# Optimization experiments

Measured on AMD Instinct MI355X. Metric: run time of the kernel, lower is better.

## Reference

```python
import jax, jax.numpy as jnp
import numpy as np

EMBED_DIM = 512
NUM_HEADS = 8
NUM_LAYERS = 2
LN_EPS = 1e-5


def setup_inputs() -> dict:
    key = jax.random.key(0)
    ks = jax.random.split(key, 12)
    B, S, E, L = 8, 1024, EMBED_DIM, NUM_LAYERS
    scale = 1.0 / np.sqrt(E)  # kaiming-ish init scale for 1x1 conv weights
    return {
        "x": jax.random.normal(ks[0], (B, S, E), jnp.float32),
        "adj": jax.random.uniform(ks[1], (S, S), jnp.float32),
        "Wq": jax.random.normal(ks[2], (L, E, E), jnp.float32) * scale,
        "bq": jnp.zeros((L, E), jnp.float32),
        "Wk": jax.random.normal(ks[3], (L, E, E), jnp.float32) * scale,
        "bk": jnp.zeros((L, E), jnp.float32),
        "Wv": jax.random.normal(ks[4], (L, E, E), jnp.float32) * scale,
        "bv": jnp.zeros((L, E), jnp.float32),
        "Wo": jax.random.normal(ks[5], (L, E, E), jnp.float32) * scale,
        "bo": jnp.zeros((L, E), jnp.float32),
        "gamma": jnp.ones((L, E), jnp.float32),
        "beta": jnp.zeros((L, E), jnp.float32),
    }


def _layer_norm(x, g, b):
    mu = jnp.mean(x, axis=-1, keepdims=True)
    var = jnp.mean(jnp.square(x - mu), axis=-1, keepdims=True)
    return (x - mu) * jax.lax.rsqrt(var + LN_EPS) * g + b


def reference(x, adj, Wq, bq, Wk, bk, Wv, bv, Wo, bo, gamma, beta):
    B, S, E = x.shape
    H = NUM_HEADS
    D = E // H
    inv_sqrt_d = 1.0 / np.sqrt(D)
    for l in range(Wq.shape[0]):
        # 1x1 Conv2d over channel dim == per-token linear: out_f = sum_e W[f,e] x_e + b_f
        q = (jnp.einsum('bse,fe->bsf', x, Wq[l]) + bq[l]).reshape(B, S, H, D).transpose(0, 2, 1, 3)
        k = (jnp.einsum('bse,fe->bsf', x, Wk[l]) + bk[l]).reshape(B, S, H, D).transpose(0, 2, 1, 3)
        v = (jnp.einsum('bse,fe->bsf', x, Wv[l]) + bv[l]).reshape(B, S, H, D).transpose(0, 2, 1, 3)
        # adjacency-gated scaled dot-product attention: multiplicative mask BEFORE softmax
        scores = jnp.einsum('bhqd,bhkd->bhqk', q, k) * inv_sqrt_d
        scores = scores * adj  # broadcast [S,S] over [B,H,S,S]
        attn = jax.nn.softmax(scores, axis=-1)
        out = jnp.einsum('bhqk,bhkd->bhqd', attn, v)
        out = out.transpose(0, 2, 1, 3).reshape(B, S, E)
        out = jnp.einsum('bse,fe->bsf', out, Wo[l]) + bo[l]
        x = _layer_norm(x + out, gamma[l], beta[l])
    return x
```

## Files before the change

### kernel.cpp

```cpp
#include <hip/hip_runtime.h>
#include <stdint.h>

typedef _Float16 f16;
typedef _Float16 f16x8 __attribute__((ext_vector_type(8)));
typedef _Float16 f16x4 __attribute__((ext_vector_type(4)));
typedef float f32x4 __attribute__((ext_vector_type(4)));

constexpr int EMB = 512;
constexpr int SEQ = 1024;
constexpr int NH = 8;
constexpr int DHEAD = 64;
constexpr int NTOK = 8192;

#define GAS __attribute__((address_space(1)))
#define LAS __attribute__((address_space(3)))

#if __has_builtin(__builtin_amdgcn_exp2f)
#define EXP2F(x) __builtin_amdgcn_exp2f(x)
#else
#define EXP2F(x) exp2f(x)
#endif

#define SCHED_BAR() __builtin_amdgcn_sched_barrier(0)

static __device__ __forceinline__ void gload_lds16(const void* g, void* l) {
  __builtin_amdgcn_global_load_lds((const GAS void*)g, (LAS void*)l, 16, 0, 0);
}


__global__ void k_pack_w(const float* __restrict__ Wq, const float* __restrict__ Wk,
                         const float* __restrict__ Wv, const float* __restrict__ Wo,
                         f16* __restrict__ wqkv, f16* __restrict__ wo) {
  int tid = blockIdx.x * 256 + threadIdx.x;
  if (tid < 2 * 1536 * 128) {
    int e4 = tid & 127;
    int f = (tid >> 7) % 1536;
    int l = tid / (128 * 1536);
    int part = f >> 9, fr = f & 511;
    const float* src = (part == 0 ? Wq : part == 1 ? Wk : Wv) + (size_t)l * EMB * EMB + (size_t)fr * EMB + e4 * 4;
    float4 v = *(const float4*)src;
    f16x4 hv = {(f16)v.x, (f16)v.y, (f16)v.z, (f16)v.w};
    *(f16x4*)(wqkv + ((size_t)l * 1536 + f) * EMB + e4 * 4) = hv;
  }
  if (tid < 2 * 512 * 128) {
    int e4 = tid & 127;
    int f = (tid >> 7) % 512;
    int l = tid / (128 * 512);
    float4 v = *(const float4*)(Wo + (size_t)l * EMB * EMB + (size_t)f * EMB + e4 * 4);
    f16x4 hv = {(f16)v.x, (f16)v.y, (f16)v.z, (f16)v.w};
    *(f16x4*)(wo + ((size_t)l * 512 + f) * EMB + e4 * 4) = hv;
  }
}

__global__ void k_pack_b(const float* __restrict__ bq, const float* __restrict__ bk,
                         const float* __restrict__ bv, float* __restrict__ bqkv) {
  int tid = blockIdx.x * 256 + threadIdx.x;
  if (tid < 2 * 1536) {
    int f = tid % 1536, l = tid / 1536;
    int part = f >> 9, fr = f & 511;
    bqkv[tid] = (part == 0 ? bq : part == 1 ? bk : bv)[l * EMB + fr];
  }
}

__global__ void k_cvt(const float* __restrict__ x, f16* __restrict__ out) {
  int i = (blockIdx.x * 256 + threadIdx.x) * 8;
  float4 a = *(const float4*)(x + i);
  float4 b = *(const float4*)(x + i + 4);
  f16x8 h = {(f16)a.x, (f16)a.y, (f16)a.z, (f16)a.w, (f16)b.x, (f16)b.y, (f16)b.z, (f16)b.w};
  *(f16x8*)(out + i) = h;
}

__global__ void k_pack_adjP(const float* __restrict__ adj, f16* __restrict__ adjP) {
  int tid = blockIdx.x * 256 + threadIdx.x;
  int lo = tid & 15, t = (tid >> 4) & 15, qrow = tid >> 8;
  const float c = 0.125f * 1.44269504088896f;
  const float* row = adj + (size_t)qrow * SEQ + t * 64 + lo;
  f16x4 v = {(f16)(row[0] * c), (f16)(row[16] * c), (f16)(row[32] * c), (f16)(row[48] * c)};
  *(f16x4*)(adjP + (size_t)tid * 4) = v;
}


template <int MODE, int BK>
__global__ __launch_bounds__(256) void k_gemm(const f16* __restrict__ A, const f16* __restrict__ Bw,
                                              const float* __restrict__ bias, f16* __restrict__ Uout,
                                              f16* __restrict__ Qo, f16* __restrict__ Ko,
                                              f16* __restrict__ Vt) {
  constexpr int CH = 128 * BK / 8;
  constexpr int NT = EMB / BK;
  __shared__ f16x8 sA[3][CH];
  __shared__ f16x8 sB[3][CH];
  const int tid = threadIdx.x;
  const int lane = tid & 63;
  const int lanelow = lane & 15, lanehi = lane >> 4;
  const int wave = tid >> 6;
  const int wm = wave >> 1, wn = wave & 1;
  const int flat = blockIdx.x;
  const int mt = (flat & 7) * 8 + ((flat >> 3) & 7);
  const int nt = flat >> 6;
  const int m0 = mt * 128, n0 = nt * 128;

  f32x4 acc[4][4] = {};

  const f16* aB = A + (size_t)m0 * EMB;
  const f16* bB = Bw + (size_t)n0 * EMB;

  int srow[4], scl[4];
#pragma unroll
  for (int p = 0; p < (BK == 64 ? 4 : 2); ++p) {
    int c = p * 256 + tid;
    if (BK == 64) {
      srow[p] = c >> 3;
      scl[p] = (c & 7) ^ (srow[p] & 7);
    } else {
      int R = c >> 3, sub = c & 7;
      srow[p] = R * 2 + (sub >> 2);
      scl[p] = (sub & 3) ^ (R & 3);
    }
  }

#define GSTAGE(ktv, bufv)                                                                     \
  {                                                                                           \
    _Pragma("unroll") for (int p = 0; p < (BK == 64 ? 4 : 2); ++p) {                          \
      int c = p * 256 + tid;                                                                  \
      gload_lds16(aB + (size_t)srow[p] * EMB + (ktv) + scl[p] * 8, (char*)sA[bufv] + c * 16); \
      gload_lds16(bB + (size_t)srow[p] * EMB + (ktv) + scl[p] * 8, (char*)sB[bufv] + c * 16); \
    }                                                                                         \
  }

  GSTAGE(0, 0);

  int cur = 0;
  for (int t = 0; t < NT; ++t) {
    const int nb = (cur == 2) ? 0 : cur + 1;
    if (t < NT - 1) GSTAGE((t + 1) * BK, nb);
    SCHED_BAR();
    if (t < NT - 1) {
      if (BK == 64) asm volatile("s_waitcnt vmcnt(8)");
      else          asm volatile("s_waitcnt vmcnt(4)");
    } else {
      asm volatile("s_waitcnt vmcnt(0)");
    }
    SCHED_BAR();
    __builtin_amdgcn_s_barrier();
    SCHED_BAR();

    const f16x8* sAc = sA[cur];
    const f16x8* sBc = sB[cur];
#pragma unroll
    for (int ks = 0; ks < BK / 32; ++ks) {
      f16x8 af[4], bf[4];
#pragma unroll
      for (int m = 0; m < 4; ++m) {
        int r = wm * 64 + m * 16 + lanelow;
        af[m] = (BK == 64) ? sAc[r * 8 + ((ks * 4 + lanehi) ^ (r & 7))]
                           : sAc[(r >> 1) * 8 + (r & 1) * 4 + (lanehi ^ ((r >> 1) & 3))];
      }
#pragma unroll
      for (int n = 0; n < 4; ++n) {
        int r = wn * 64 + n * 16 + lanelow;
        bf[n] = (BK == 64) ? sBc[r * 8 + ((ks * 4 + lanehi) ^ (r & 7))]
                           : sBc[(r >> 1) * 8 + (r & 1) * 4 + (lanehi ^ ((r >> 1) & 3))];
      }
      __builtin_amdgcn_s_setprio(1);
#pragma unroll
      for (int m = 0; m < 4; ++m)
#pragma unroll
        for (int n = 0; n < 4; ++n)
          acc[m][n] = __builtin_amdgcn_mfma_f32_16x16x32_f16(af[m], bf[n], acc[m][n], 0, 0, 0);
      __builtin_amdgcn_s_setprio(0);
    }
    cur = nb;
  }
#undef GSTAGE

#pragma unroll
  for (int n = 0; n < 4; ++n) {
    int col = n0 + wn * 64 + n * 16 + lanelow;
    float bv = bias[col];
    if (MODE == 1 && (col >> 9) == 2) {
      int fr = col & 511, hh = fr >> 6, d = fr & 63;
#pragma unroll
      for (int m = 0; m < 4; ++m) {
        int rbase = m0 + wm * 64 + m * 16 + lanehi * 4;
        int b = rbase >> 10, s = rbase & 1023;
        f16x4 pv = {(f16)(acc[m][n][0] + bv), (f16)(acc[m][n][1] + bv),
                    (f16)(acc[m][n][2] + bv), (f16)(acc[m][n][3] + bv)};
        *(f16x4*)(Vt + ((size_t)(b * NH + hh) * DHEAD + d) * SEQ + s) = pv;
      }
    } else {
#pragma unroll
      for (int m = 0; m < 4; ++m) {
        int rbase = m0 + wm * 64 + m * 16 + lanehi * 4;
#pragma unroll
        for (int j = 0; j < 4; ++j) {
          float v = acc[m][n][j] + bv;
          int row = rbase + j;
          if (MODE == 0) {
            Uout[(size_t)row * EMB + col] = (f16)v;
          } else {
            int part = col >> 9, fr = col & 511;
            int hh = fr >> 6, d = fr & 63;
            int b = row >> 10, s = row & 1023;
            int bh = b * NH + hh;
            if (part == 0)
              Qo[((size_t)bh * SEQ + s) * DHEAD + d] = (f16)v;
            else
              Ko[((size_t)bh * SEQ + s) * DHEAD + d] = (f16)v;
          }
        }
      }
    }
  }
}


__global__ __launch_bounds__(256, 4) void k_attn(const f16* __restrict__ Q, const f16* __restrict__ K,
                                                 const f16* __restrict__ Vt, const f16* __restrict__ adjP,
                                                 f16* __restrict__ Ob) {
  __shared__ __align__(16) f16 sK[2][4096];
  __shared__ __align__(16) f16 sV[2][4096];
  __shared__ __align__(16) f16 Pl[4 * 1024];
  const int tid = threadIdx.x;
  const int lane = tid & 63;
  const int lanelow = lane & 15, lanehi = lane >> 4;
  const int wave = tid >> 6;
  f16* Plw = Pl + wave * 1024;

  const int flat = blockIdx.x;
  const int bh = (flat & 7) * 8 + ((flat >> 3) & 7);
  const int qblk = flat >> 6;
  const int b = bh >> 3, hh = bh & 7;
  const int q0 = qblk * 64 + wave * 16;

  const f16* Kbase = K + (size_t)bh * SEQ * DHEAD;
  const f16* Vbase = Vt + (size_t)bh * DHEAD * SEQ;

  const int c0 = tid, c1 = tid + 256;
  const int r0 = c0 >> 3, ch0 = (c0 & 7) ^ (r0 & 7);
  const int r1 = c1 >> 3, ch1 = (c1 & 7) ^ (r1 & 7);

#define STAGE(tv, bufv)                                                                   \
  {                                                                                       \
    const int kts = (tv)*64;                                                              \
    gload_lds16(Kbase + (size_t)(kts + r0) * DHEAD + ch0 * 8, (char*)sK[bufv] + c0 * 16); \
    gload_lds16(Kbase + (size_t)(kts + r1) * DHEAD + ch1 * 8, (char*)sK[bufv] + c1 * 16); \
    gload_lds16(Vbase + (size_t)r0 * SEQ + kts + ch0 * 8, (char*)sV[bufv] + c0 * 16);     \
    gload_lds16(Vbase + (size_t)r1 * SEQ + kts + ch1 * 8, (char*)sV[bufv] + c1 * 16);     \
  }

  f16x8 qf[2];
#pragma unroll
  for (int ks = 0; ks < 2; ++ks)
    qf[ks] = *(const f16x8*)(Q + ((size_t)bh * SEQ + q0 + lanelow) * DHEAD + ks * 32 + lanehi * 8);

  const f16* Ab = adjP + ((size_t)(q0 + lanehi * 4) * 256 + lanelow) * 4;
  f16x4 ab[4];
#define LOAD_A(tv)                                                           \
  {                                                                          \
    _Pragma("unroll") for (int j = 0; j < 4; ++j)                            \
        ab[j] = *(const f16x4*)(Ab + ((size_t)j * 256 + (tv)*16) * 4);       \
  }

  f32x4 oacc[4] = {};
  float lpart[4] = {};

  STAGE(0, 0);
  LOAD_A(0);
  __syncthreads();

  int cur = 0;
  for (int t = 0; t < 16; ++t) {
    if (t < 15) STAGE(t + 1, cur ^ 1);

    const f16* sKc = sK[cur];
    const f16* sVc = sV[cur];

    f32x4 sacc[4] = {};
#pragma unroll
    for (int ks = 0; ks < 2; ++ks) {
      f16x8 kf[4];
#pragma unroll
      for (int n = 0; n < 4; ++n) {
        int r = n * 16 + lanelow;
        kf[n] = *(const f16x8*)(sKc + (r * 8 + ((ks * 4 + lanehi) ^ (r & 7))) * 8);
      }
      __builtin_amdgcn_s_setprio(1);
#pragma unroll
      for (int n = 0; n < 4; ++n)
        sacc[n] = __builtin_amdgcn_mfma_f32_16x16x32_f16(qf[ks], kf[n], sacc[n], 0, 0, 0);
      __builtin_amdgcn_s_setprio(0);
    }

    f16x4 acur[4];
#pragma unroll
    for (int j = 0; j < 4; ++j) acur[j] = ab[j];
    if (t < 15) LOAD_A(t + 1);

#pragma unroll
    for (int nh = 0; nh < 2; ++nh) {
#pragma unroll
      for (int j = 0; j < 4; ++j) {
        const int prow = lanehi * 4 + j;
        const f16x4 a4 = acur[j];
#pragma unroll
        for (int nn = 0; nn < 2; ++nn) {
          const int n = nh * 2 + nn;
          float p = EXP2F(sacc[n][j] * (float)a4[n]);
          lpart[j] += p;
          Plw[prow * 64 + (((n * 2 + (lanelow >> 3)) ^ (prow & 7)) * 8) + (lanelow & 7)] = (f16)p;
        }
      }
      f16x8 pa, vf[4];
      pa = *(const f16x8*)(Plw + lanelow * 64 + (((nh * 4 + lanehi) ^ (lanelow & 7)) * 8));
#pragma unroll
      for (int n = 0; n < 4; ++n) {
        int r = n * 16 + lanelow;
        vf[n] = *(const f16x8*)(sVc + (r * 8 + ((nh * 4 + lanehi) ^ (r & 7))) * 8);
      }
      __builtin_amdgcn_s_setprio(1);
#pragma unroll
      for (int n = 0; n < 4; ++n)
        oacc[n] = __builtin_amdgcn_mfma_f32_16x16x32_f16(pa, vf[n], oacc[n], 0, 0, 0);
      __builtin_amdgcn_s_setprio(0);
    }

    __syncthreads();
    cur ^= 1;
  }
#undef STAGE
#undef LOAD_A

  float linv[4];
#pragma unroll
  for (int j = 0; j < 4; ++j) {
    float l = lpart[j];
#pragma unroll
    for (int off = 1; off < 16; off <<= 1) l += __shfl_xor(l, off, 16);
    linv[j] = 1.0f / l;
  }
#pragma unroll
  for (int n = 0; n < 4; ++n)
#pragma unroll
    for (int j = 0; j < 4; ++j) {
      int qrow = q0 + lanehi * 4 + j;
      float v = oacc[n][j] * linv[j];
      Ob[((size_t)b * SEQ + qrow) * EMB + hh * DHEAD + n * 16 + lanelow] = (f16)v;
    }
}


__global__ __launch_bounds__(256) void k_ln(const float* __restrict__ xin, const f16* __restrict__ Uin,
                                            const float* __restrict__ gamma, const float* __restrict__ beta,
                                            float* __restrict__ xout, f16* __restrict__ xh_out) {
  const int row = blockIdx.x * 4 + (threadIdx.x >> 6);
  const int lane = threadIdx.x & 63;
  const size_t base = (size_t)row * EMB + lane * 8;
  float u[8];
  {
    float4 a0 = *(const float4*)(xin + base);
    float4 a1 = *(const float4*)(xin + base + 4);
    f16x8 uh = *(const f16x8*)(Uin + base);
    u[0] = a0.x + (float)uh[0]; u[1] = a0.y + (float)uh[1];
    u[2] = a0.z + (float)uh[2]; u[3] = a0.w + (float)uh[3];
    u[4] = a1.x + (float)uh[4]; u[5] = a1.y + (float)uh[5];
    u[6] = a1.z + (float)uh[6]; u[7] = a1.w + (float)uh[7];
  }
  float s = 0.f;
#pragma unroll
  for (int i = 0; i < 8; ++i) s += u[i];
#pragma unroll
  for (int off = 1; off < 64; off <<= 1) s += __shfl_xor(s, off, 64);
  const float mu = s * (1.0f / EMB);
  float v = 0.f;
#pragma unroll
  for (int i = 0; i < 8; ++i) { float d = u[i] - mu; v += d * d; }
#pragma unroll
  for (int off = 1; off < 64; off <<= 1) v += __shfl_xor(v, off, 64);
  const float rs = rsqrtf(v * (1.0f / EMB) + 1e-5f);
  const int ci = lane * 8;
  float4 g0 = *(const float4*)(gamma + ci);
  float4 g1 = *(const float4*)(gamma + ci + 4);
  float4 b0 = *(const float4*)(beta + ci);
  float4 b1 = *(const float4*)(beta + ci + 4);
  float g[8] = {g0.x, g0.y, g0.z, g0.w, g1.x, g1.y, g1.z, g1.w};
  float be[8] = {b0.x, b0.y, b0.z, b0.w, b1.x, b1.y, b1.z, b1.w};
  float o[8];
#pragma unroll
  for (int i = 0; i < 8; ++i) o[i] = (u[i] - mu) * rs * g[i] + be[i];
  float4 o0 = {o[0], o[1], o[2], o[3]}, o1 = {o[4], o[5], o[6], o[7]};
  *(float4*)(xout + base) = o0;
  *(float4*)(xout + base + 4) = o1;
  if (xh_out) {
    f16x8 hv = {(f16)o[0], (f16)o[1], (f16)o[2], (f16)o[3], (f16)o[4], (f16)o[5], (f16)o[6], (f16)o[7]};
    *(f16x8*)(xh_out + base) = hv;
  }
}


extern "C" void kernel_launch(void* const* d_in, const int* in_sizes, int n_in,
                              void* d_out, int out_size, void* d_ws, size_t ws_size,
                              hipStream_t stream) {
  (void)in_sizes; (void)n_in; (void)out_size; (void)ws_size;
  const float* x = (const float*)d_in[0];
  const float* adj = (const float*)d_in[1];
  const float* Wq = (const float*)d_in[2];
  const float* bq = (const float*)d_in[3];
  const float* Wk = (const float*)d_in[4];
  const float* bk = (const float*)d_in[5];
  const float* Wv = (const float*)d_in[6];
  const float* bv = (const float*)d_in[7];
  const float* Wo = (const float*)d_in[8];
  const float* bo = (const float*)d_in[9];
  const float* gamma = (const float*)d_in[10];
  const float* beta = (const float*)d_in[11];

  char* ws = (char*)d_ws;
  size_t off = 0;
  auto alloc = [&](size_t bytes) {
    char* p = ws + off;
    off += (bytes + 255) & ~(size_t)255;
    return p;
  };
  f16* wqkv = (f16*)alloc((size_t)2 * 1536 * 512 * sizeof(f16));
  f16* wo = (f16*)alloc((size_t)2 * 512 * 512 * sizeof(f16));
  float* bqkv = (float*)alloc((size_t)2 * 1536 * sizeof(float));
  f16* adjP = (f16*)alloc((size_t)SEQ * SEQ * sizeof(f16));
  f16* xh = (f16*)alloc((size_t)NTOK * EMB * sizeof(f16));
  f16* Qb = (f16*)alloc((size_t)NTOK * EMB * sizeof(f16));
  f16* Kb = (f16*)alloc((size_t)NTOK * EMB * sizeof(f16));
  f16* Vtb = (f16*)alloc((size_t)NTOK * EMB * sizeof(f16));
  f16* Ob = (f16*)alloc((size_t)NTOK * EMB * sizeof(f16));
  f16* U = (f16*)alloc((size_t)NTOK * EMB * sizeof(f16));
  float* x1 = (float*)alloc((size_t)NTOK * EMB * sizeof(float));

  k_pack_w<<<1536, 256, 0, stream>>>(Wq, Wk, Wv, Wo, wqkv, wo);
  k_pack_b<<<12, 256, 0, stream>>>(bq, bk, bv, bqkv);
  k_pack_adjP<<<1024, 256, 0, stream>>>(adj, adjP);
  k_cvt<<<2048, 256, 0, stream>>>(x, xh);

  const float* xcur = x;
  for (int l = 0; l < 2; ++l) {
    k_gemm<1, 32><<<768, 256, 0, stream>>>(xh, wqkv + (size_t)l * 1536 * 512, bqkv + l * 1536,
                                           nullptr, Qb, Kb, Vtb);
    k_attn<<<1024, 256, 0, stream>>>(Qb, Kb, Vtb, adjP, Ob);
    k_gemm<0, 64><<<256, 256, 0, stream>>>(Ob, wo + (size_t)l * 512 * 512, bo + l * 512,
                                           U, nullptr, nullptr, nullptr);
    float* xnext = (l == 0) ? x1 : (float*)d_out;
    k_ln<<<2048, 256, 0, stream>>>(xcur, U, gamma + l * 512, beta + l * 512, xnext,
                                   (l == 0) ? xh : nullptr);
    xcur = xnext;
  }
}
```

Before: 172.7 us.

## Prefetch GEMM tiles two stages ahead and keep layer-1 residual in fp16

```diff
diff --git a/kernel.cpp b/kernel.cpp
--- a/kernel.cpp
+++ b/kernel.cpp
@@ -128,11 +128,10 @@
   }
 
   GSTAGE(0, 0);
+  GSTAGE(BK, 1);
 
   int cur = 0;
   for (int t = 0; t < NT; ++t) {
-    const int nb = (cur == 2) ? 0 : cur + 1;
-    if (t < NT - 1) GSTAGE((t + 1) * BK, nb);
     SCHED_BAR();
     if (t < NT - 1) {
       if (BK == 64) asm volatile("s_waitcnt vmcnt(8)");
@@ -143,6 +142,7 @@
     SCHED_BAR();
     __builtin_amdgcn_s_barrier();
     SCHED_BAR();
+    if (t < NT - 2) GSTAGE((t + 2) * BK, (cur == 0) ? 2 : cur - 1);
 
     const f16x8* sAc = sA[cur];
     const f16x8* sBc = sB[cur];
@@ -169,7 +169,7 @@
           acc[m][n] = __builtin_amdgcn_mfma_f32_16x16x32_f16(af[m], bf[n], acc[m][n], 0, 0, 0);
       __builtin_amdgcn_s_setprio(0);
     }
-    cur = nb;
+    cur = (cur == 2) ? 0 : cur + 1;
   }
 #undef GSTAGE
 
@@ -349,7 +349,9 @@
 }
 
 
-__global__ __launch_bounds__(256) void k_ln(const float* __restrict__ xin, const f16* __restrict__ Uin,
+template <int INH>
+__global__ __launch_bounds__(256) void k_ln(const float* __restrict__ xf, const f16* __restrict__ xh_in,
+                                            const f16* __restrict__ Uin,
                                             const float* __restrict__ gamma, const float* __restrict__ beta,
                                             float* __restrict__ xout, f16* __restrict__ xh_out) {
   const int row = blockIdx.x * 4 + (threadIdx.x >> 6);
@@ -357,13 +359,19 @@
   const size_t base = (size_t)row * EMB + lane * 8;
   float u[8];
   {
-    float4 a0 = *(const float4*)(xin + base);
-    float4 a1 = *(const float4*)(xin + base + 4);
     f16x8 uh = *(const f16x8*)(Uin + base);
-    u[0] = a0.x + (float)uh[0]; u[1] = a0.y + (float)uh[1];
-    u[2] = a0.z + (float)uh[2]; u[3] = a0.w + (float)uh[3];
-    u[4] = a1.x + (float)uh[4]; u[5] = a1.y + (float)uh[5];
-    u[6] = a1.z + (float)uh[6]; u[7] = a1.w + (float)uh[7];
+    if (INH) {
+      f16x8 xh8 = *(const f16x8*)(xh_in + base);
+#pragma unroll
+      for (int i = 0; i < 8; ++i) u[i] = (float)xh8[i] + (float)uh[i];
+    } else {
+      float4 a0 = *(const float4*)(xf + base);
+      float4 a1 = *(const float4*)(xf + base + 4);
+      u[0] = a0.x + (float)uh[0]; u[1] = a0.y + (float)uh[1];
+      u[2] = a0.z + (float)uh[2]; u[3] = a0.w + (float)uh[3];
+      u[4] = a1.x + (float)uh[4]; u[5] = a1.y + (float)uh[5];
+      u[6] = a1.z + (float)uh[6]; u[7] = a1.w + (float)uh[7];
+    }
   }
   float s = 0.f;
 #pragma unroll
@@ -387,9 +395,11 @@
   float o[8];
 #pragma unroll
   for (int i = 0; i < 8; ++i) o[i] = (u[i] - mu) * rs * g[i] + be[i];
-  float4 o0 = {o[0], o[1], o[2], o[3]}, o1 = {o[4], o[5], o[6], o[7]};
-  *(float4*)(xout + base) = o0;
-  *(float4*)(xout + base + 4) = o1;
+  if (xout) {
+    float4 o0 = {o[0], o[1], o[2], o[3]}, o1 = {o[4], o[5], o[6], o[7]};
+    *(float4*)(xout + base) = o0;
+    *(float4*)(xout + base + 4) = o1;
+  }
   if (xh_out) {
     f16x8 hv = {(f16)o[0], (f16)o[1], (f16)o[2], (f16)o[3], (f16)o[4], (f16)o[5], (f16)o[6], (f16)o[7]};
     *(f16x8*)(xh_out + base) = hv;
@@ -431,23 +441,21 @@
   f16* Vtb = (f16*)alloc((size_t)NTOK * EMB * sizeof(f16));
   f16* Ob = (f16*)alloc((size_t)NTOK * EMB * sizeof(f16));
   f16* U = (f16*)alloc((size_t)NTOK * EMB * sizeof(f16));
-  float* x1 = (float*)alloc((size_t)NTOK * EMB * sizeof(float));
 
   k_pack_w<<<1536, 256, 0, stream>>>(Wq, Wk, Wv, Wo, wqkv, wo);
   k_pack_b<<<12, 256, 0, stream>>>(bq, bk, bv, bqkv);
   k_pack_adjP<<<1024, 256, 0, stream>>>(adj, adjP);
   k_cvt<<<2048, 256, 0, stream>>>(x, xh);
 
-  const float* xcur = x;
   for (int l = 0; l < 2; ++l) {
     k_gemm<1, 32><<<768, 256, 0, stream>>>(xh, wqkv + (size_t)l * 1536 * 512, bqkv + l * 1536,
                                            nullptr, Qb, Kb, Vtb);
     k_attn<<<1024, 256, 0, stream>>>(Qb, Kb, Vtb, adjP, Ob);
     k_gemm<0, 64><<<256, 256, 0, stream>>>(Ob, wo + (size_t)l * 512 * 512, bo + l * 512,
                                            U, nullptr, nullptr, nullptr);
-    float* xnext = (l == 0) ? x1 : (float*)d_out;
-    k_ln<<<2048, 256, 0, stream>>>(xcur, U, gamma + l * 512, beta + l * 512, xnext,
-                                   (l == 0) ? xh : nullptr);
-    xcur = xnext;
-  }
-}
+    if (l == 0)
+      k_ln<0><<<2048, 256, 0, stream>>>(x, nullptr, U, gamma, beta, nullptr, xh);
+    else
+      k_ln<1><<<2048, 256, 0, stream>>>(nullptr, xh, U, gamma + 512, beta + 512, (float*)d_out, nullptr);
+  }
+}
```

Measured after the change: 171.1 us. No clear change (-0.9%).
